# Optimization experiments

Measured on AMD Instinct MI355X. Metric: run time of the kernel, lower is better.

The kernel has to match this reference:

```python
import jax, jax.numpy as jnp
import numpy as np

NUM_TIME_BLOCKS = 32  # P
B, L, D = 32, 4096, 256


def setup_inputs() -> dict:
    key = jax.random.key(0)
    k1, k2 = jax.random.split(key)
    x = jax.random.normal(k1, (B, L, D), dtype=jnp.float32)
    # normalized timestamps in [0, 1), matching linspace(0, 1.001, P+1) bin edges
    time_steps = jax.random.uniform(k2, (B, L), dtype=jnp.float32)
    return {"x": x, "time_steps": time_steps}


def reference(x, time_steps):
    # Bin edges identical to torch.linspace(0.0, 1.001, P+1)
    blocks = jnp.linspace(0.0, 1.001, NUM_TIME_BLOCKS + 1, dtype=jnp.float32)
    ls = blocks[:-1]  # (P,) left edges (inclusive)
    rs = blocks[1:]   # (P,) right edges (exclusive)
    ts = time_steps[..., None]                      # (B, L, 1)
    # one-hot bucket membership mask, (B, L, P); a token falls in exactly one bin
    mask = ((ts >= ls) & (ts < rs)).astype(x.dtype)
    # sum x over sequence positions within each time bucket -> (B, P, D)
    new_x = jnp.einsum('blp,bld->bpd', mask, x)
    return new_x, time_steps
```

## Files before the change

kernel.cpp:

```cpp
#include <hip/hip_runtime.h>


#define Bk 32
#define Lk 4096
#define Dk 256
#define Pk 32
#define NRS 16
#define RB (Lk / NRS)
#define NTH 512
#define NW 8
#define UN 8

typedef float v4f __attribute__((ext_vector_type(4)));

__device__ __forceinline__ int bucket_of(float tv) {
    const double step = 1.001 / 32.0;
    int p = (int)(tv * (float)(32.0 / 1.001));
    p = p < 0 ? 0 : (p > 31 ? 31 : p);
    while (p > 0 && tv < (float)((double)p * step)) --p;
    while (p < 31 && tv >= (float)((double)(p + 1) * step)) ++p;
    return p;
}

__global__ __launch_bounds__(NTH, 4) void tc_fx(
        const float* __restrict__ x,
        const float* __restrict__ ts,
        float* __restrict__ out,
        float* __restrict__ ts_out) {
    __shared__ int acc[4 * Pk * 64];
    __shared__ unsigned char pbuf[RB];

    const int rs = blockIdx.x;
    const int b  = blockIdx.y;
    const int t  = threadIdx.x;
    const int w  = t >> 6;
    const int lane = t & 63;

    {
        v4f z = 0.f;
#pragma unroll
        for (int i = t; i < 4 * Pk * 64 / 4; i += NTH) ((v4f*)acc)[i] = z;
    }

    if (t < RB) {
        const size_t li = (size_t)b * Lk + (size_t)rs * RB + t;
        const float tv = ts[li];
        ts_out[li] = tv;
        pbuf[t] = (unsigned char)bucket_of(tv);
    }
    __syncthreads();

    const float* xb = x + ((size_t)b * Lk + (size_t)rs * RB) * Dk + (lane << 2);
    const float S = 32768.0f;

    for (int i0 = 0; i0 < RB / NW; i0 += UN) {
        v4f v[UN];
        int pu[UN];
#pragma unroll
        for (int u = 0; u < UN; ++u) {
            const int r = (i0 + u) * NW + w;
            v[u] = __builtin_nontemporal_load((const v4f*)(xb + (size_t)r * Dk));
            pu[u] = pbuf[r];
        }
#pragma unroll
        for (int u = 0; u < UN; ++u) {
            const int base = (pu[u] << 6) + lane;
            atomicAdd(&acc[base       ], __float2int_rn(v[u].x * S));
            atomicAdd(&acc[base + 2048], __float2int_rn(v[u].y * S));
            atomicAdd(&acc[base + 4096], __float2int_rn(v[u].z * S));
            atomicAdd(&acc[base + 6144], __float2int_rn(v[u].w * S));
        }
    }
    __syncthreads();

    const float IS = 1.0f / 32768.0f;
    float* ob = out + (size_t)b * Pk * Dk;
#pragma unroll
    for (int e = t; e < Pk * Dk; e += NTH) {
        const int p = e >> 8;
        const int c = e & 255;
        const int iv = acc[((c & 3) << 11) + (p << 6) + (c >> 2)];
        unsafeAtomicAdd(ob + e, (float)iv * IS);
    }
}

extern "C" void kernel_launch(void* const* d_in, const int* in_sizes, int n_in,
                              void* d_out, int out_size, void* d_ws, size_t ws_size,
                              hipStream_t stream) {
    const float* x  = (const float*)d_in[0];
    const float* ts = (const float*)d_in[1];
    float* out = (float*)d_out;
    float* ts_out = out + (size_t)Bk * Pk * Dk;

    hipMemsetAsync(out, 0, (size_t)Bk * Pk * Dk * sizeof(float), stream);
    dim3 grid(NRS, Bk);
    tc_fx<<<grid, NTH, 0, stream>>>(x, ts, out, ts_out);
}
```

Before: 188.8 us.

## Stream x rows through per-wave LDS ring via async global_load_lds

Replaces register-batched nontemporal loads with an 8-deep per-wave LDS ring filled by global_load_lds, using explicit vmcnt waits so global loads overlap the LDS atomic accumulation. Halves the grid to 8 segments per batch (512 rows per block, 256 blocks), sets launch bounds to one block per SM, and raises the fixed-point scale to 65536. The aim is to keep more loads in flight per wave while cutting register pressure and the number of output atomic flushes. Risks include lower occupancy, fewer blocks than the GPU has CUs, reliance on hand-written vmcnt counts being correct, and a higher chance of int32 overflow with the larger scale.

```diff
diff --git a/kernel.cpp b/kernel.cpp
--- a/kernel.cpp
+++ b/kernel.cpp
@@ -5,13 +5,16 @@
 #define Lk 4096
 #define Dk 256
 #define Pk 32
-#define NRS 16
-#define RB (Lk / NRS)
+#define NSEG 8
+#define RB (Lk / NSEG)
 #define NTH 512
 #define NW 8
-#define UN 8
+#define RING 8
+#define RPW (RB / NW)
 
 typedef float v4f __attribute__((ext_vector_type(4)));
+typedef const __attribute__((address_space(1))) void* gas_t;
+typedef __attribute__((address_space(3))) void* las_t;
 
 __device__ __forceinline__ int bucket_of(float tv) {
     const double step = 1.001 / 32.0;
@@ -22,18 +25,19 @@
     return p;
 }
 
-__global__ __launch_bounds__(NTH, 4) void tc_fx(
+__global__ __launch_bounds__(NTH, 1) void tc_ring(
         const float* __restrict__ x,
         const float* __restrict__ ts,
         float* __restrict__ out,
         float* __restrict__ ts_out) {
+    __shared__ float ring[NW][RING][Dk];
     __shared__ int acc[4 * Pk * 64];
     __shared__ unsigned char pbuf[RB];
 
-    const int rs = blockIdx.x;
-    const int b  = blockIdx.y;
-    const int t  = threadIdx.x;
-    const int w  = t >> 6;
+    const int seg  = blockIdx.x;
+    const int b    = blockIdx.y;
+    const int t    = threadIdx.x;
+    const int w    = t >> 6;
     const int lane = t & 63;
 
     {
@@ -42,38 +46,45 @@
         for (int i = t; i < 4 * Pk * 64 / 4; i += NTH) ((v4f*)acc)[i] = z;
     }
 
-    if (t < RB) {
-        const size_t li = (size_t)b * Lk + (size_t)rs * RB + t;
+    {
+        const size_t li = (size_t)b * Lk + (size_t)seg * RB + t;
         const float tv = ts[li];
         ts_out[li] = tv;
         pbuf[t] = (unsigned char)bucket_of(tv);
     }
     __syncthreads();
 
-    const float* xb = x + ((size_t)b * Lk + (size_t)rs * RB) * Dk + (lane << 2);
-    const float S = 32768.0f;
+    const float* xb = x + ((size_t)b * Lk + (size_t)seg * RB) * Dk;
 
-    for (int i0 = 0; i0 < RB / NW; i0 += UN) {
-        v4f v[UN];
-        int pu[UN];
+    auto stage = [&](int i, int slot) {
+        const int r = i * NW + w;
+        const float* g = xb + (size_t)r * Dk + (lane << 2);
+        __builtin_amdgcn_global_load_lds((gas_t)g, (las_t)&ring[w][slot][0],
+                                         16, 0, 0);
+    };
+
 #pragma unroll
-        for (int u = 0; u < UN; ++u) {
-            const int r = (i0 + u) * NW + w;
-            v[u] = __builtin_nontemporal_load((const v4f*)(xb + (size_t)r * Dk));
-            pu[u] = pbuf[r];
-        }
-#pragma unroll
-        for (int u = 0; u < UN; ++u) {
-            const int base = (pu[u] << 6) + lane;
-            atomicAdd(&acc[base       ], __float2int_rn(v[u].x * S));
-            atomicAdd(&acc[base + 2048], __float2int_rn(v[u].y * S));
-            atomicAdd(&acc[base + 4096], __float2int_rn(v[u].z * S));
-            atomicAdd(&acc[base + 6144], __float2int_rn(v[u].w * S));
-        }
+    for (int s = 0; s < RING; ++s) stage(s, s);
+
+    const float S = 65536.0f;
+    for (int i = 0; i < RPW; ++i) {
+        const int slot = i & (RING - 1);
+        if (i < RPW - RING)       asm volatile("s_waitcnt vmcnt(7)" ::: "memory");
+        else if (i == RPW - RING) asm volatile("s_waitcnt vmcnt(0)" ::: "memory");
+
+        const int p = pbuf[i * NW + w];
+        const v4f v = *(const v4f*)&ring[w][slot][lane << 2];
+        const int base = (p << 6) + lane;
+        atomicAdd(&acc[base       ], __float2int_rn(v.x * S));
+        atomicAdd(&acc[base + 2048], __float2int_rn(v.y * S));
+        atomicAdd(&acc[base + 4096], __float2int_rn(v.z * S));
+        atomicAdd(&acc[base + 6144], __float2int_rn(v.w * S));
+        asm volatile("" ::: "memory");
+        if (i + RING < RPW) stage(i + RING, slot);
     }
     __syncthreads();
 
-    const float IS = 1.0f / 32768.0f;
+    const float IS = 1.0f / 65536.0f;
     float* ob = out + (size_t)b * Pk * Dk;
 #pragma unroll
     for (int e = t; e < Pk * Dk; e += NTH) {
@@ -93,6 +104,6 @@
     float* ts_out = out + (size_t)Bk * Pk * Dk;
 
     hipMemsetAsync(out, 0, (size_t)Bk * Pk * Dk * sizeof(float), stream);
-    dim3 grid(NRS, Bk);
-    tc_fx<<<grid, NTH, 0, stream>>>(x, ts, out, ts_out);
+    dim3 grid(NSEG, Bk);
+    tc_ring<<<grid, NTH, 0, stream>>>(x, ts, out, ts_out);
 }
```

After: 205.5 us. +8.8%, slower.
